# Kernel tuning notes

Hardware: AMD Instinct MI355X
Metric: run time of the kernel (lower is better)

The kernel has to match this reference:

```python
import jax, jax.numpy as jnp
import numpy as np

T, B, I, H = 512, 64, 1024, 1024
DROPOUT = 0.3


def setup_inputs() -> dict:
    key = jax.random.key(0)
    k = jax.random.split(key, 6)
    s = 1.0 / np.sqrt(H).astype(np.float32)
    x = jax.random.normal(k[0], (T, B, I), dtype=jnp.float32)
    w_ih = jax.random.uniform(k[1], (4 * H, I), minval=-s, maxval=s, dtype=jnp.float32)
    w_hh = jax.random.uniform(k[2], (4 * H, H), minval=-s, maxval=s, dtype=jnp.float32)
    b_ih = jax.random.uniform(k[3], (4 * H,), minval=-s, maxval=s, dtype=jnp.float32)
    b_hh = jax.random.uniform(k[4], (4 * H,), minval=-s, maxval=s, dtype=jnp.float32)
    # init_weights: forget-gate bias (second quarter) set to 1
    b_ih = b_ih.at[H:2 * H].set(1.0)
    b_hh = b_hh.at[H:2 * H].set(1.0)
    # DropConnect mask on recurrent weights (training-mode dropout, fixed realization)
    keep = jax.random.bernoulli(k[5], 1.0 - DROPOUT, (4 * H, H))
    hh_mask = keep.astype(jnp.float32) / (1.0 - DROPOUT)
    return {"x": x, "w_ih": w_ih, "w_hh": w_hh, "b_ih": b_ih, "b_hh": b_hh, "hh_mask": hh_mask}


def reference(x, w_ih, w_hh, b_ih, b_hh, hh_mask):
    # x: (T, B, I). PyTorch LSTM gate order: i, f, g, o.
    h = w_hh.shape[1]
    w_hh_dropped = w_hh * hh_mask  # DropConnect applied once per forward
    # Precompute input contribution for all timesteps (one big GEMM): (T, B, 4H)
    gx = jnp.einsum('tbi,gi->tbg', x, w_ih) + b_ih + b_hh

    def step(carry, g_t):
        h_t, c_t = carry
        gates = g_t + h_t @ w_hh_dropped.T  # (B, 4H)
        i_g, f_g, g_g, o_g = jnp.split(gates, 4, axis=-1)
        i_g = jax.nn.sigmoid(i_g)
        f_g = jax.nn.sigmoid(f_g)
        g_g = jnp.tanh(g_g)
        o_g = jax.nn.sigmoid(o_g)
        c_new = f_g * c_t + i_g * g_g
        h_new = o_g * jnp.tanh(c_new)
        return (h_new, c_new), h_new

    bsz = x.shape[1]
    init = (jnp.zeros((bsz, h), x.dtype), jnp.zeros((bsz, h), x.dtype))
    (hn, cn), out = jax.lax.scan(step, init, gx)
    # match torch: output (T,B,H), hn/cn with leading num_layers dim
    return out, hn[None], cn[None]
```

## Files before the change

### kernel.cpp

```cpp
#include <hip/hip_runtime.h>

#define TT 512
#define BB 64
#define II 1024
#define HH 1024
#define GG 4096
#define BH 65536
#define NBLK 128

typedef __attribute__((ext_vector_type(8))) short bf16x8;
typedef __attribute__((ext_vector_type(4))) float f32x4;
typedef __attribute__((ext_vector_type(4))) unsigned u32x4;

__device__ __forceinline__ float bf2f(unsigned short u) {
  union { unsigned int i; float f; } v; v.i = ((unsigned int)u) << 16; return v.f;
}
__device__ __forceinline__ unsigned short f2bf(float f) {
  union { float f; unsigned int i; } v; v.f = f;
  return (unsigned short)((v.i + 0x7FFFu + ((v.i >> 16) & 1u)) >> 16);
}
__device__ __forceinline__ bf16x8 pack8(float4 a, float4 b) {
  union { bf16x8 v; unsigned short u[8]; } p;
  p.u[0] = f2bf(a.x); p.u[1] = f2bf(a.y); p.u[2] = f2bf(a.z); p.u[3] = f2bf(a.w);
  p.u[4] = f2bf(b.x); p.u[5] = f2bf(b.y); p.u[6] = f2bf(b.z); p.u[7] = f2bf(b.w);
  return p.v;
}
__device__ __forceinline__ float sigmoid_f(float x) { return 1.0f / (1.0f + __expf(-x)); }
__device__ __forceinline__ float tanh_f(float x) {
  float e = __expf(-2.0f * fabsf(x));
  float t = (1.0f - e) / (1.0f + e);
  return copysignf(t, x);
}

__device__ __forceinline__ void st32_uc(unsigned* p, unsigned v) {
  __hip_atomic_store(p, v, __ATOMIC_RELAXED, __HIP_MEMORY_SCOPE_AGENT);
}
__device__ __forceinline__ unsigned ld32_uc(const unsigned* p) {
  return __hip_atomic_load(p, __ATOMIC_RELAXED, __HIP_MEMORY_SCOPE_AGENT);
}
__device__ __forceinline__ void st128_uc(void* p, u32x4 v) {
  asm volatile("global_store_dwordx4 %0, %1, off sc0 sc1" :: "v"(p), "v"(v) : "memory");
}
__device__ __forceinline__ void lds_add_rel(int* p) {
  __hip_atomic_fetch_add(p, 1, __ATOMIC_RELEASE, __HIP_MEMORY_SCOPE_WORKGROUP);
}
__device__ __forceinline__ int lds_ld_acq(const int* p) {
  return __hip_atomic_load(p, __ATOMIC_ACQUIRE, __HIP_MEMORY_SCOPE_WORKGROUP);
}
__device__ __forceinline__ void lds_st_rel(int* p, int v) {
  __hip_atomic_store(p, v, __ATOMIC_RELEASE, __HIP_MEMORY_SCOPE_WORKGROUP);
}

__global__ __launch_bounds__(256) void wdlstm_xconv(
    const float* __restrict__ xc, unsigned short* __restrict__ xbf, int n4) {
  int stride = gridDim.x * blockDim.x;
  for (int i = blockIdx.x * blockDim.x + threadIdx.x; i < n4; i += stride) {
    float4 v = *(const float4*)(xc + (size_t)i * 4);
    unsigned short o[4] = {f2bf(v.x), f2bf(v.y), f2bf(v.z), f2bf(v.w)};
    *(unsigned long long*)(xbf + (size_t)i * 4) = *(unsigned long long*)o;
  }
}

__global__ __launch_bounds__(512) void wdlstm_fused(
    const float* __restrict__ w_hh, const float* __restrict__ hh_mask,
    const float* __restrict__ w_ih,
    const float* __restrict__ b_ih, const float* __restrict__ b_hh,
    const unsigned short* __restrict__ xbf,
    float* __restrict__ out, float* __restrict__ c_state,
    unsigned* __restrict__ flags,
    unsigned short* __restrict__ hinit,
    unsigned short* __restrict__ hring,
    int t0, int tc) {
  __shared__ __align__(16) char Wh[65536];
  __shared__ __align__(16) char Wi[65536];
  __shared__ float Dw[4][16][33];
  __shared__ __align__(8) unsigned short Dgx[4][32][72];
  __shared__ __align__(16) unsigned Hsw[4][16][4];
  __shared__ int syncv[8];

  const int tid = threadIdx.x;
  const int wv  = tid >> 6, l = tid & 63;
  const int ln  = l & 15, lq = l >> 4;
  const int j0h = blockIdx.x * 8;

  for (int c = tid; c < 4096; c += 512) {
    int n = c >> 7, cc = c & 127;
    int wrow = (n >> 3) * HH + j0h + (n & 7);
    int addr = (n * 2048 + cc * 16) ^ ((n & 7) << 4);
    {
      const float* sw = w_hh   + (size_t)wrow * HH + cc * 8;
      const float* sm = hh_mask + (size_t)wrow * HH + cc * 8;
      float4 w0 = *(const float4*)sw, w1 = *(const float4*)(sw + 4);
      float4 m0 = *(const float4*)sm, m1 = *(const float4*)(sm + 4);
      float4 p0 = {w0.x * m0.x, w0.y * m0.y, w0.z * m0.z, w0.w * m0.w};
      float4 p1 = {w1.x * m1.x, w1.y * m1.y, w1.z * m1.z, w1.w * m1.w};
      *(bf16x8*)(Wh + addr) = pack8(p0, p1);
    }
    {
      const float* si = w_ih + (size_t)wrow * II + cc * 8;
      float4 a0 = *(const float4*)si, a1 = *(const float4*)(si + 4);
      *(bf16x8*)(Wi + addr) = pack8(a0, a1);
    }
  }
  if (tid < 8) syncv[tid] = 0;
  __syncthreads();

  if (wv < 4) {
    const int b_ew = 16 * wv + ln;
    const int jj0  = 2 * lq;
    float c_reg[2];
    if (t0 == 0) { c_reg[0] = c_reg[1] = 0.f; }
    else {
      float2 cv = *(const float2*)(c_state + (size_t)b_ew * HH + j0h + jj0);
      c_reg[0] = cv.x; c_reg[1] = cv.y;
    }
    float biasv[4][2];
#pragma unroll
    for (int g = 0; g < 4; ++g)
#pragma unroll
      for (int q = 0; q < 2; ++q) {
        int col = g * HH + j0h + jj0 + q;
        biasv[g][q] = b_ih[col] + b_hh[col];
      }
    float* hn_out = out + (size_t)TT * BH;
    float* cn_out = hn_out + BH;

    for (int lt = 0; lt < tc; ++lt) {
      const int t = t0 + lt;
      f32x4 acc[2];
      acc[0] = (f32x4){0.f, 0.f, 0.f, 0.f};
      acc[1] = (f32x4){0.f, 0.f, 0.f, 0.f};

      if (t > 0) {
        if (lt > 0) {
          if (wv == 0) {
            const unsigned* f0 = flags + (2 * l) * 16;
            const unsigned* f1 = flags + (2 * l + 1) * 16;
            while ((int)ld32_uc(f0) < t || (int)ld32_uc(f1) < t)
              __builtin_amdgcn_s_sleep(1);
            if (l == 0) lds_st_rel(&syncv[7], t);
          } else {
            while (lds_ld_acq(&syncv[7]) < t) {}
          }
        }
        const unsigned short* hp = (lt == 0) ? hinit : hring + (size_t)(lt - 1) * BH;
        const unsigned short* ap = hp + (size_t)(16 * wv + ln) * HH + lq * 8;
        bf16x8 aA[8], aB[8];
#pragma unroll
        for (int i = 0; i < 8; ++i) aA[i] = *(const bf16x8*)(ap + i * 32);
#pragma unroll
        for (int c4 = 0; c4 < 4; ++c4) {
          const bf16x8* cur = (c4 & 1) ? aB : aA;
          bf16x8*       nxt = (c4 & 1) ? aA : aB;
          if (c4 < 3) {
#pragma unroll
            for (int i = 0; i < 8; ++i) nxt[i] = *(const bf16x8*)(ap + (c4 + 1) * 256 + i * 32);
          }
#pragma unroll
          for (int i = 0; i < 8; ++i) {
            int kc = c4 * 8 + i;
#pragma unroll
            for (int ni = 0; ni < 2; ++ni) {
              int n = 16 * ni + ln;
              int baddr = (n * 2048 + kc * 64 + lq * 16) ^ ((n & 7) << 4);
              bf16x8 b = *(const bf16x8*)(Wh + baddr);
              acc[ni] = __builtin_amdgcn_mfma_f32_16x16x32_bf16(cur[i], b, acc[ni], 0, 0, 0);
            }
          }
        }
      }
#pragma unroll
      for (int ni = 0; ni < 2; ++ni)
#pragma unroll
        for (int r = 0; r < 4; ++r)
          Dw[wv][4 * lq + r][16 * ni + ln] = acc[ni][r];

      while (lds_ld_acq(&syncv[2]) < lt + 1 || lds_ld_acq(&syncv[3]) < lt + 1 ||
             lds_ld_acq(&syncv[4]) < lt + 1 || lds_ld_acq(&syncv[5]) < lt + 1)
        __builtin_amdgcn_s_sleep(1);
      asm volatile("s_waitcnt lgkmcnt(0)" ::: "memory");

      const int slot = lt & 3;
      float hq[2];
#pragma unroll
      for (int q = 0; q < 2; ++q) {
        int jj = jj0 + q;
        float g0 = Dw[wv][ln][ 0 + jj] + bf2f(Dgx[slot][ 0 + jj][b_ew]) + biasv[0][q];
        float g1 = Dw[wv][ln][ 8 + jj] + bf2f(Dgx[slot][ 8 + jj][b_ew]) + biasv[1][q];
        float g2 = Dw[wv][ln][16 + jj] + bf2f(Dgx[slot][16 + jj][b_ew]) + biasv[2][q];
        float g3 = Dw[wv][ln][24 + jj] + bf2f(Dgx[slot][24 + jj][b_ew]) + biasv[3][q];
        float ig = sigmoid_f(g0);
        float fg = sigmoid_f(g1);
        float gg = tanh_f(g2);
        float og = sigmoid_f(g3);
        c_reg[q] = fg * c_reg[q] + ig * gg;
        hq[q] = og * tanh_f(c_reg[q]);
      }
      if (l == 0) lds_add_rel(&syncv[1]);

      *(float2*)(out + (size_t)t * BH + (size_t)b_ew * HH + j0h + jj0) = make_float2(hq[0], hq[1]);
      Hsw[wv][ln][lq] = (unsigned)f2bf(hq[0]) | ((unsigned)f2bf(hq[1]) << 16);
      if (t == TT - 1) {
        *(float2*)(hn_out + (size_t)b_ew * HH + j0h + jj0) = make_float2(hq[0], hq[1]);
        *(float2*)(cn_out + (size_t)b_ew * HH + j0h + jj0) = make_float2(c_reg[0], c_reg[1]);
      }
      asm volatile("s_waitcnt lgkmcnt(0)" ::: "memory");

      if (l < 16) {
        u32x4 hv4 = *(const u32x4*)&Hsw[wv][l][0];
        char* dst = (char*)hring + ((size_t)lt * BH + (size_t)(16 * wv + l) * HH + j0h) * 2;
        st128_uc(dst, hv4);
        if (lt == tc - 1)
          *(u32x4*)((char*)hinit + ((size_t)(16 * wv + l) * HH + j0h) * 2) = hv4;
      }
      asm volatile("s_waitcnt vmcnt(0)" ::: "memory");
      if (l == 0) lds_add_rel(&syncv[6]);
      if (wv == 0) {
        const int tgt = 4 * (lt + 1);
        while (lds_ld_acq(&syncv[6]) < tgt) {}
        if (l == 0) st32_uc(&flags[blockIdx.x * 16], (unsigned)(t + 1));
      }
    }
    *(float2*)(c_state + (size_t)b_ew * HH + j0h + jj0) = make_float2(c_reg[0], c_reg[1]);

  } else {
    const int w2 = wv - 4;
    for (int s = 0; s < tc; ++s) {
      if (s >= 4) {
        const int tgt = 4 * (s - 3);
        while (lds_ld_acq(&syncv[1]) < tgt) __builtin_amdgcn_s_sleep(1);
      }
      f32x4 acc[2];
      acc[0] = (f32x4){0.f, 0.f, 0.f, 0.f};
      acc[1] = (f32x4){0.f, 0.f, 0.f, 0.f};
      const unsigned short* ap = xbf + (size_t)s * BH + (size_t)(16 * w2 + ln) * II + lq * 8;
      bf16x8 aA[8], aB[8];
#pragma unroll
      for (int i = 0; i < 8; ++i) aA[i] = *(const bf16x8*)(ap + i * 32);
#pragma unroll
      for (int c4 = 0; c4 < 4; ++c4) {
        const bf16x8* cur = (c4 & 1) ? aB : aA;
        bf16x8*       nxt = (c4 & 1) ? aA : aB;
        if (c4 < 3) {
#pragma unroll
          for (int i = 0; i < 8; ++i) nxt[i] = *(const bf16x8*)(ap + (c4 + 1) * 256 + i * 32);
        }
#pragma unroll
        for (int i = 0; i < 8; ++i) {
          int kc = c4 * 8 + i;
#pragma unroll
          for (int ni = 0; ni < 2; ++ni) {
            int n = 16 * ni + ln;
            int baddr = (n * 2048 + kc * 64 + lq * 16) ^ ((n & 7) << 4);
            bf16x8 b = *(const bf16x8*)(Wi + baddr);
            acc[ni] = __builtin_amdgcn_mfma_f32_16x16x32_bf16(cur[i], b, acc[ni], 0, 0, 0);
          }
        }
      }
      const int slot = s & 3;
#pragma unroll
      for (int ni = 0; ni < 2; ++ni) {
        unsigned short p[4] = {f2bf(acc[ni][0]), f2bf(acc[ni][1]),
                               f2bf(acc[ni][2]), f2bf(acc[ni][3])};
        *(unsigned long long*)&Dgx[slot][16 * ni + ln][16 * w2 + 4 * lq] =
            *(unsigned long long*)p;
      }
      if (l == 0) lds_st_rel(&syncv[2 + w2], s + 1);
    }
  }
}

extern "C" void kernel_launch(void* const* d_in, const int* in_sizes, int n_in,
                              void* d_out, int out_size, void* d_ws, size_t ws_size,
                              hipStream_t stream) {
  const float* x       = (const float*)d_in[0];
  const float* w_ih    = (const float*)d_in[1];
  const float* w_hh    = (const float*)d_in[2];
  const float* b_ih    = (const float*)d_in[3];
  const float* b_hh    = (const float*)d_in[4];
  const float* hh_mask = (const float*)d_in[5];
  float* out           = (float*)d_out;

  char* ws = (char*)d_ws;
  float* c_state        = (float*)ws;
  unsigned* flags       = (unsigned*)(ws + 262144);
  unsigned short* hinit = (unsigned short*)(ws + 270336);
  unsigned short* hring = (unsigned short*)(ws + 401408);

  const long long fixed = 401408;
  const long long per_t = 131072 + 131072;
  long long avail = (long long)ws_size - fixed;
  int TC = (int)(avail / per_t);
  if (TC > TT) TC = TT;
  if (TC < 2) TC = 2;
  unsigned short* xbf = (unsigned short*)(ws + 401408 + (size_t)TC * 131072);

  hipMemsetAsync(flags, 0, 8192, stream);

  for (int t0 = 0; t0 < TT; t0 += TC) {
    int tc = TT - t0 < TC ? TT - t0 : TC;
    const float* xc = x + (size_t)t0 * BB * II;
    wdlstm_xconv<<<256, 256, 0, stream>>>(xc, xbf, tc * BH / 4);
    wdlstm_fused<<<NBLK, 512, 0, stream>>>(w_hh, hh_mask, w_ih, b_ih, b_hh, xbf,
                                           out, c_state, flags, hinit, hring, t0, tc);
  }
}
```

Measured before the change: 4.640 ms.

## Keep weight slices in registers and split recurrent GEMM along K across waves

Recurrent and input weight tiles now live in VGPRs instead of LDS. Each wave owns a quarter of the K dimension and covers all 64 batch rows, and the partial sums are reduced through LDS before the gate math. The gx ring shrinks to two slots, the compute waves raise their priority, and the conversion kernel gets more blocks. The goal is to remove per-step LDS weight reads and shorten the serial recurrence step, at the cost of heavy register pressure and an extra reduction with its own intra-block sync.

Measured after the change: 5.016 ms. 1.08x slower.

```diff
diff --git a/kernel.cpp b/kernel.cpp
--- a/kernel.cpp
+++ b/kernel.cpp
@@ -71,11 +71,10 @@
     unsigned short* __restrict__ hinit,
     unsigned short* __restrict__ hring,
     int t0, int tc) {
-  __shared__ __align__(16) char Wh[65536];
-  __shared__ __align__(16) char Wi[65536];
-  __shared__ float Dw[4][16][33];
-  __shared__ __align__(8) unsigned short Dgx[4][32][72];
-  __shared__ __align__(16) unsigned Hsw[4][16][4];
+  __shared__ float Dpart[4][64][33];
+  __shared__ unsigned short Dgx[2][4][32][72];
+  __shared__ __align__(16) unsigned Hs[64][4];
+  __shared__ float bias_lds[32];
   __shared__ int syncv[8];
 
   const int tid = threadIdx.x;
@@ -83,53 +82,52 @@
   const int ln  = l & 15, lq = l >> 4;
   const int j0h = blockIdx.x * 8;
 
-  for (int c = tid; c < 4096; c += 512) {
-    int n = c >> 7, cc = c & 127;
-    int wrow = (n >> 3) * HH + j0h + (n & 7);
-    int addr = (n * 2048 + cc * 16) ^ ((n & 7) << 4);
-    {
-      const float* sw = w_hh   + (size_t)wrow * HH + cc * 8;
-      const float* sm = hh_mask + (size_t)wrow * HH + cc * 8;
-      float4 w0 = *(const float4*)sw, w1 = *(const float4*)(sw + 4);
-      float4 m0 = *(const float4*)sm, m1 = *(const float4*)(sm + 4);
-      float4 p0 = {w0.x * m0.x, w0.y * m0.y, w0.z * m0.z, w0.w * m0.w};
-      float4 p1 = {w1.x * m1.x, w1.y * m1.y, w1.z * m1.z, w1.w * m1.w};
-      *(bf16x8*)(Wh + addr) = pack8(p0, p1);
-    }
-    {
-      const float* si = w_ih + (size_t)wrow * II + cc * 8;
-      float4 a0 = *(const float4*)si, a1 = *(const float4*)(si + 4);
-      *(bf16x8*)(Wi + addr) = pack8(a0, a1);
-    }
+  if (tid < 8) syncv[tid] = 0;
+  if (tid < 32) {
+    int gcol = (tid >> 3) * HH + j0h + (tid & 7);
+    bias_lds[tid] = b_ih[gcol] + b_hh[gcol];
   }
-  if (tid < 8) syncv[tid] = 0;
   __syncthreads();
 
   if (wv < 4) {
-    const int b_ew = 16 * wv + ln;
-    const int jj0  = 2 * lq;
+    __builtin_amdgcn_s_setprio(1);
+    const int kq = wv;
+    const int b_ew = l;
+    const int jj0  = 2 * wv;
+
+    bf16x8 Bh[2][8];
+#pragma unroll
+    for (int ni = 0; ni < 2; ++ni)
+#pragma unroll
+      for (int kc = 0; kc < 8; ++kc) {
+        int n = 16 * ni + ln;
+        int wrow = (n >> 3) * HH + j0h + (n & 7);
+        int k0 = kq * 256 + kc * 32 + lq * 8;
+        const float* sw = w_hh   + (size_t)wrow * HH + k0;
+        const float* sm = hh_mask + (size_t)wrow * HH + k0;
+        float4 w0 = *(const float4*)sw, w1 = *(const float4*)(sw + 4);
+        float4 m0 = *(const float4*)sm, m1 = *(const float4*)(sm + 4);
+        float4 p0 = {w0.x * m0.x, w0.y * m0.y, w0.z * m0.z, w0.w * m0.w};
+        float4 p1 = {w1.x * m1.x, w1.y * m1.y, w1.z * m1.z, w1.w * m1.w};
+        Bh[ni][kc] = pack8(p0, p1);
+      }
+
     float c_reg[2];
     if (t0 == 0) { c_reg[0] = c_reg[1] = 0.f; }
     else {
       float2 cv = *(const float2*)(c_state + (size_t)b_ew * HH + j0h + jj0);
       c_reg[0] = cv.x; c_reg[1] = cv.y;
     }
-    float biasv[4][2];
-#pragma unroll
-    for (int g = 0; g < 4; ++g)
-#pragma unroll
-      for (int q = 0; q < 2; ++q) {
-        int col = g * HH + j0h + jj0 + q;
-        biasv[g][q] = b_ih[col] + b_hh[col];
-      }
     float* hn_out = out + (size_t)TT * BH;
     float* cn_out = hn_out + BH;
 
     for (int lt = 0; lt < tc; ++lt) {
       const int t = t0 + lt;
-      f32x4 acc[2];
-      acc[0] = (f32x4){0.f, 0.f, 0.f, 0.f};
-      acc[1] = (f32x4){0.f, 0.f, 0.f, 0.f};
+      f32x4 acc[4][2];
+#pragma unroll
+      for (int mi = 0; mi < 4; ++mi)
+#pragma unroll
+        for (int ni = 0; ni < 2; ++ni) acc[mi][ni] = (f32x4){0.f, 0.f, 0.f, 0.f};
 
       if (t > 0) {
         if (lt > 0) {
@@ -143,81 +141,83 @@
             while (lds_ld_acq(&syncv[7]) < t) {}
           }
         }
-        const unsigned short* hp = (lt == 0) ? hinit : hring + (size_t)(lt - 1) * BH;
-        const unsigned short* ap = hp + (size_t)(16 * wv + ln) * HH + lq * 8;
-        bf16x8 aA[8], aB[8];
-#pragma unroll
-        for (int i = 0; i < 8; ++i) aA[i] = *(const bf16x8*)(ap + i * 32);
-#pragma unroll
-        for (int c4 = 0; c4 < 4; ++c4) {
-          const bf16x8* cur = (c4 & 1) ? aB : aA;
-          bf16x8*       nxt = (c4 & 1) ? aA : aB;
-          if (c4 < 3) {
-#pragma unroll
-            for (int i = 0; i < 8; ++i) nxt[i] = *(const bf16x8*)(ap + (c4 + 1) * 256 + i * 32);
-          }
-#pragma unroll
-          for (int i = 0; i < 8; ++i) {
-            int kc = c4 * 8 + i;
-#pragma unroll
-            for (int ni = 0; ni < 2; ++ni) {
-              int n = 16 * ni + ln;
-              int baddr = (n * 2048 + kc * 64 + lq * 16) ^ ((n & 7) << 4);
-              bf16x8 b = *(const bf16x8*)(Wh + baddr);
-              acc[ni] = __builtin_amdgcn_mfma_f32_16x16x32_bf16(cur[i], b, acc[ni], 0, 0, 0);
-            }
-          }
+        const char* hpb = (lt == 0) ? (const char*)hinit
+                                    : (const char*)(hring + (size_t)(lt - 1) * BH);
+        const char* base = hpb + ((size_t)ln * 1024 + kq * 256 + lq * 8) * 2;
+#pragma unroll
+        for (int h = 0; h < 2; ++h) {
+          bf16x8 A[2][8];
+#pragma unroll
+          for (int m2 = 0; m2 < 2; ++m2)
+#pragma unroll
+            for (int kc = 0; kc < 8; ++kc)
+              A[m2][kc] = *(const bf16x8*)(base + (size_t)(h * 2 + m2) * 32768 + kc * 64);
+#pragma unroll
+          for (int kc = 0; kc < 8; ++kc)
+#pragma unroll
+            for (int m2 = 0; m2 < 2; ++m2)
+#pragma unroll
+              for (int ni = 0; ni < 2; ++ni)
+                acc[h * 2 + m2][ni] = __builtin_amdgcn_mfma_f32_16x16x32_bf16(
+                    A[m2][kc], Bh[ni][kc], acc[h * 2 + m2][ni], 0, 0, 0);
         }
       }
 #pragma unroll
-      for (int ni = 0; ni < 2; ++ni)
-#pragma unroll
-        for (int r = 0; r < 4; ++r)
-          Dw[wv][4 * lq + r][16 * ni + ln] = acc[ni][r];
-
-      while (lds_ld_acq(&syncv[2]) < lt + 1 || lds_ld_acq(&syncv[3]) < lt + 1 ||
-             lds_ld_acq(&syncv[4]) < lt + 1 || lds_ld_acq(&syncv[5]) < lt + 1)
-        __builtin_amdgcn_s_sleep(1);
-      asm volatile("s_waitcnt lgkmcnt(0)" ::: "memory");
-
-      const int slot = lt & 3;
+      for (int mi = 0; mi < 4; ++mi)
+#pragma unroll
+        for (int ni = 0; ni < 2; ++ni)
+#pragma unroll
+          for (int r = 0; r < 4; ++r)
+            Dpart[kq][16 * mi + 4 * lq + r][16 * ni + ln] = acc[mi][ni][r];
+      if (l == 0) lds_add_rel(&syncv[0]);
+      {
+        const int tgt = 4 * (lt + 1);
+        while (lds_ld_acq(&syncv[0]) < tgt) {}
+        while (lds_ld_acq(&syncv[2]) < lt + 1 || lds_ld_acq(&syncv[3]) < lt + 1 ||
+               lds_ld_acq(&syncv[4]) < lt + 1 || lds_ld_acq(&syncv[5]) < lt + 1)
+          __builtin_amdgcn_s_sleep(1);
+      }
+
+      const int slot = lt & 1;
       float hq[2];
 #pragma unroll
       for (int q = 0; q < 2; ++q) {
         int jj = jj0 + q;
-        float g0 = Dw[wv][ln][ 0 + jj] + bf2f(Dgx[slot][ 0 + jj][b_ew]) + biasv[0][q];
-        float g1 = Dw[wv][ln][ 8 + jj] + bf2f(Dgx[slot][ 8 + jj][b_ew]) + biasv[1][q];
-        float g2 = Dw[wv][ln][16 + jj] + bf2f(Dgx[slot][16 + jj][b_ew]) + biasv[2][q];
-        float g3 = Dw[wv][ln][24 + jj] + bf2f(Dgx[slot][24 + jj][b_ew]) + biasv[3][q];
-        float ig = sigmoid_f(g0);
-        float fg = sigmoid_f(g1);
-        float gg = tanh_f(g2);
-        float og = sigmoid_f(g3);
+        float gs[4];
+#pragma unroll
+        for (int g = 0; g < 4; ++g) {
+          int n = g * 8 + jj;
+          float s = bias_lds[n];
+#pragma unroll
+          for (int k2 = 0; k2 < 4; ++k2) s += Dpart[k2][b_ew][n];
+#pragma unroll
+          for (int k2 = 0; k2 < 4; ++k2) s += bf2f(Dgx[slot][k2][n][b_ew]);
+          gs[g] = s;
+        }
+        float ig = sigmoid_f(gs[0]);
+        float fg = sigmoid_f(gs[1]);
+        float gg = tanh_f(gs[2]);
+        float og = sigmoid_f(gs[3]);
         c_reg[q] = fg * c_reg[q] + ig * gg;
         hq[q] = og * tanh_f(c_reg[q]);
       }
-      if (l == 0) lds_add_rel(&syncv[1]);
-
       *(float2*)(out + (size_t)t * BH + (size_t)b_ew * HH + j0h + jj0) = make_float2(hq[0], hq[1]);
-      Hsw[wv][ln][lq] = (unsigned)f2bf(hq[0]) | ((unsigned)f2bf(hq[1]) << 16);
+      Hs[b_ew][wv] = (unsigned)f2bf(hq[0]) | ((unsigned)f2bf(hq[1]) << 16);
       if (t == TT - 1) {
         *(float2*)(hn_out + (size_t)b_ew * HH + j0h + jj0) = make_float2(hq[0], hq[1]);
         *(float2*)(cn_out + (size_t)b_ew * HH + j0h + jj0) = make_float2(c_reg[0], c_reg[1]);
       }
-      asm volatile("s_waitcnt lgkmcnt(0)" ::: "memory");
-
-      if (l < 16) {
-        u32x4 hv4 = *(const u32x4*)&Hsw[wv][l][0];
-        char* dst = (char*)hring + ((size_t)lt * BH + (size_t)(16 * wv + l) * HH + j0h) * 2;
+      if (l == 0) lds_add_rel(&syncv[1]);
+
+      if (wv == 0) {
+        const int tgt = 4 * (lt + 1);
+        while (lds_ld_acq(&syncv[1]) < tgt) {}
+        u32x4 hv4 = *(const u32x4*)&Hs[l][0];
+        char* dst = (char*)hring + ((size_t)lt * BH + (size_t)l * HH + j0h) * 2;
         st128_uc(dst, hv4);
         if (lt == tc - 1)
-          *(u32x4*)((char*)hinit + ((size_t)(16 * wv + l) * HH + j0h) * 2) = hv4;
-      }
-      asm volatile("s_waitcnt vmcnt(0)" ::: "memory");
-      if (l == 0) lds_add_rel(&syncv[6]);
-      if (wv == 0) {
-        const int tgt = 4 * (lt + 1);
-        while (lds_ld_acq(&syncv[6]) < tgt) {}
+          *(u32x4*)((char*)hinit + ((size_t)l * HH + j0h) * 2) = hv4;
+        asm volatile("s_waitcnt vmcnt(0)" ::: "memory");
         if (l == 0) st32_uc(&flags[blockIdx.x * 16], (unsigned)(t + 1));
       }
     }
@@ -225,46 +225,58 @@
 
   } else {
     const int w2 = wv - 4;
+    bf16x8 Bi[2][8];
+#pragma unroll
+    for (int ni = 0; ni < 2; ++ni)
+#pragma unroll
+      for (int kc = 0; kc < 8; ++kc) {
+        int n = 16 * ni + ln;
+        int wrow = (n >> 3) * HH + j0h + (n & 7);
+        int k0 = w2 * 256 + kc * 32 + lq * 8;
+        const float* si = w_ih + (size_t)wrow * II + k0;
+        float4 a0 = *(const float4*)si, a1 = *(const float4*)(si + 4);
+        Bi[ni][kc] = pack8(a0, a1);
+      }
+
     for (int s = 0; s < tc; ++s) {
-      if (s >= 4) {
-        const int tgt = 4 * (s - 3);
+      if (s >= 2) {
+        const int tgt = 4 * (s - 1);
         while (lds_ld_acq(&syncv[1]) < tgt) __builtin_amdgcn_s_sleep(1);
       }
-      f32x4 acc[2];
-      acc[0] = (f32x4){0.f, 0.f, 0.f, 0.f};
-      acc[1] = (f32x4){0.f, 0.f, 0.f, 0.f};
-      const unsigned short* ap = xbf + (size_t)s * BH + (size_t)(16 * w2 + ln) * II + lq * 8;
-      bf16x8 aA[8], aB[8];
-#pragma unroll
-      for (int i = 0; i < 8; ++i) aA[i] = *(const bf16x8*)(ap + i * 32);
-#pragma unroll
-      for (int c4 = 0; c4 < 4; ++c4) {
-        const bf16x8* cur = (c4 & 1) ? aB : aA;
-        bf16x8*       nxt = (c4 & 1) ? aA : aB;
-        if (c4 < 3) {
-#pragma unroll
-          for (int i = 0; i < 8; ++i) nxt[i] = *(const bf16x8*)(ap + (c4 + 1) * 256 + i * 32);
+      f32x4 acc[4][2];
+#pragma unroll
+      for (int mi = 0; mi < 4; ++mi)
+#pragma unroll
+        for (int ni = 0; ni < 2; ++ni) acc[mi][ni] = (f32x4){0.f, 0.f, 0.f, 0.f};
+      const char* base = (const char*)xbf + (size_t)s * BH * 2
+                         + ((size_t)ln * 1024 + w2 * 256 + lq * 8) * 2;
+#pragma unroll
+      for (int h = 0; h < 2; ++h) {
+        bf16x8 A[2][8];
+#pragma unroll
+        for (int m2 = 0; m2 < 2; ++m2)
+#pragma unroll
+          for (int kc = 0; kc < 8; ++kc)
+            A[m2][kc] = *(const bf16x8*)(base + (size_t)(h * 2 + m2) * 32768 + kc * 64);
+#pragma unroll
+        for (int kc = 0; kc < 8; ++kc)
+#pragma unroll
+          for (int m2 = 0; m2 < 2; ++m2)
+#pragma unroll
+            for (int ni = 0; ni < 2; ++ni)
+              acc[h * 2 + m2][ni] = __builtin_amdgcn_mfma_f32_16x16x32_bf16(
+                  A[m2][kc], Bi[ni][kc], acc[h * 2 + m2][ni], 0, 0, 0);
+      }
+      const int slot = s & 1;
+#pragma unroll
+      for (int mi = 0; mi < 4; ++mi)
+#pragma unroll
+        for (int ni = 0; ni < 2; ++ni) {
+          unsigned short p[4] = {f2bf(acc[mi][ni][0]), f2bf(acc[mi][ni][1]),
+                                 f2bf(acc[mi][ni][2]), f2bf(acc[mi][ni][3])};
+          *(unsigned long long*)&Dgx[slot][w2][16 * ni + ln][16 * mi + 4 * lq] =
+              *(unsigned long long*)p;
         }
-#pragma unroll
-        for (int i = 0; i < 8; ++i) {
-          int kc = c4 * 8 + i;
-#pragma unroll
-          for (int ni = 0; ni < 2; ++ni) {
-            int n = 16 * ni + ln;
-            int baddr = (n * 2048 + kc * 64 + lq * 16) ^ ((n & 7) << 4);
-            bf16x8 b = *(const bf16x8*)(Wi + baddr);
-            acc[ni] = __builtin_amdgcn_mfma_f32_16x16x32_bf16(cur[i], b, acc[ni], 0, 0, 0);
-          }
-        }
-      }
-      const int slot = s & 3;
-#pragma unroll
-      for (int ni = 0; ni < 2; ++ni) {
-        unsigned short p[4] = {f2bf(acc[ni][0]), f2bf(acc[ni][1]),
-                               f2bf(acc[ni][2]), f2bf(acc[ni][3])};
-        *(unsigned long long*)&Dgx[slot][16 * ni + ln][16 * w2 + 4 * lq] =
-            *(unsigned long long*)p;
-      }
       if (l == 0) lds_st_rel(&syncv[2 + w2], s + 1);
     }
   }
@@ -300,7 +312,7 @@
   for (int t0 = 0; t0 < TT; t0 += TC) {
     int tc = TT - t0 < TC ? TT - t0 : TC;
     const float* xc = x + (size_t)t0 * BB * II;
-    wdlstm_xconv<<<256, 256, 0, stream>>>(xc, xbf, tc * BH / 4);
+    wdlstm_xconv<<<1024, 256, 0, stream>>>(xc, xbf, tc * BH / 4);
     wdlstm_fused<<<NBLK, 512, 0, stream>>>(w_hh, hh_mask, w_ih, b_ih, b_hh, xbf,
                                            out, c_state, flags, hinit, hring, t0, tc);
   }
```
